# Kernel optimization log

Measured on AMD Instinct MI355X. Metric: run time of the kernel, lower is better.

## Reference

```python
import jax, jax.numpy as jnp
import numpy as np

K = 3          # kernel_size
PAD = K // 2   # unfold padding
BN_EPS = 1e-5


def _conv(x, w, dilation, pad):
    # x: [B,C,H,W], w: [O,I,kh,kw]
    return jax.lax.conv_general_dilated(
        x, w, window_strides=(1, 1), padding=[(pad, pad), (pad, pad)],
        rhs_dilation=(dilation, dilation),
        dimension_numbers=("NCHW", "OIHW", "NCHW"))


def _bn(x, g, b, rm, rv):
    # eval-mode batchnorm with running stats
    inv = g / jnp.sqrt(rv + BN_EPS)
    return x * inv[None, :, None, None] + (b - rm * inv)[None, :, None, None]


def setup_inputs() -> dict:
    key = jax.random.key(0)
    ks = jax.random.split(key, 8)
    B, T, H, W = 8, 5, 512, 512
    mid = 16  # max(16, T // 4)
    inp = {
        "x_aligned": jax.random.normal(ks[0], (B, T, H, W), jnp.float32),
        "raw_diff": jax.random.normal(ks[1], (B, T - 1, H, W), jnp.float32),
        "w1": jax.random.normal(ks[2], (mid, T, 3, 3), jnp.float32) * 0.1,
        "g1": jnp.ones((mid,), jnp.float32), "b1": jnp.zeros((mid,), jnp.float32),
        "rm1": jnp.zeros((mid,), jnp.float32), "rv1": jnp.ones((mid,), jnp.float32),
        "w2": jax.random.normal(ks[3], (mid, mid, 3, 3), jnp.float32) * 0.1,
        "g2": jnp.ones((mid,), jnp.float32), "b2": jnp.zeros((mid,), jnp.float32),
        "rm2": jnp.zeros((mid,), jnp.float32), "rv2": jnp.ones((mid,), jnp.float32),
        "w3": jax.random.normal(ks[4], (mid, mid, 3, 3), jnp.float32) * 0.1,
        "g3": jnp.ones((mid,), jnp.float32), "b3": jnp.zeros((mid,), jnp.float32),
        "rm3": jnp.zeros((mid,), jnp.float32), "rv3": jnp.ones((mid,), jnp.float32),
        "w4": jax.random.normal(ks[5], (T * K * K, mid, 1, 1), jnp.float32) * 0.1,
        "bias": jnp.full((1,), -1.0, jnp.float32),
    }
    return inp


def reference(x_aligned, raw_diff, w1, g1, b1, rm1, rv1, w2, g2, b2, rm2, rv2,
              w3, g3, b3, rm3, rv3, w4, bias):
    B, T, H, W = x_aligned.shape
    # _accumulate: sequential abs-add == sum of abs over frame-diff axis
    acc = jnp.sum(jnp.abs(raw_diff), axis=1, keepdims=True)  # [B,1,H,W]
    mean = jnp.mean(acc)
    n = acc.size
    std = jnp.sqrt(jnp.sum((acc - mean) ** 2) / (n - 1))  # unbiased (torch default)
    motion = (acc - mean) / (std + 1e-6)
    motion_seq = jnp.broadcast_to(motion, (B, T, H, W))
    # _generate_kernel: conv+BN+ReLU stack with dilations 1,2,4 then 1x1
    h = jax.nn.relu(_bn(_conv(motion_seq, w1, 1, 1), g1, b1, rm1, rv1))
    h = jax.nn.relu(_bn(_conv(h, w2, 2, 2), g2, b2, rm2, rv2))
    h = jax.nn.relu(_bn(_conv(h, w3, 4, 4), g3, b3, rm3, rv3))
    raw_kernel = _conv(h, w4, 1, 0).reshape(B, T, K * K, H, W)
    kernel = (jax.nn.sigmoid(raw_kernel + bias[0]) + 0.01) * 10.0
    # _enhance: unfold (KxK patches, zero pad) then per-pixel weighted sum
    xp = jnp.pad(x_aligned, ((0, 0), (0, 0), (PAD, PAD), (PAD, PAD)))
    patches = jnp.stack(
        [xp[:, :, i:i + H, j:j + W] for i in range(K) for j in range(K)],
        axis=2)  # [B,T,K*K,H,W], matches F.unfold row-major kernel order
    return jnp.sum(kernel * patches, axis=2)  # [B,T,H,W]
```

## Files before the change

kernel.cpp:

```cpp
#include <hip/hip_runtime.h>
#include <hip/hip_bf16.h>
#include <math.h>

#define HH 512
#define WW 512
#define BB 8
#define TT 5
#define MID 16
#define HWSZ (HH*WW)
#define NPIX (BB*HWSZ)

typedef __attribute__((ext_vector_type(8))) short bf16x8;
typedef __attribute__((ext_vector_type(4))) float f32x4;

__device__ inline unsigned short f2bf(float f){
  unsigned u = __float_as_uint(f);
  u = u + 0x7fffu + ((u >> 16) & 1u);
  return (unsigned short)(u >> 16);
}
__device__ inline unsigned packpair(float a, float b){
  unsigned ua = __float_as_uint(a) + 0x8000u;
  unsigned ub = __float_as_uint(b) + 0x8000u;
  return __builtin_amdgcn_perm(ub, ua, 0x07060302u);
}
__device__ inline float blo(unsigned u){ return __uint_as_float(u << 16); }
__device__ inline float bhi(unsigned u){ return __uint_as_float(u & 0xffff0000u); }

union U4B { uint4 u; bf16x8 h; };


__global__ __launch_bounds__(256) void k_acc(const float* __restrict__ rd,
                                             float4* __restrict__ acc,
                                             float2* __restrict__ partial){
  int t = blockIdx.x * 256 + threadIdx.x;
  int i = t << 2;
  int b = i >> 18, p = i & (HWSZ - 1);
  const float* base = rd + (size_t)b * 4 * HWSZ + p;
  float4 f0 = *(const float4*)(base);
  float4 f1 = *(const float4*)(base + HWSZ);
  float4 f2 = *(const float4*)(base + 2*HWSZ);
  float4 f3 = *(const float4*)(base + 3*HWSZ);
  float4 s4;
  s4.x = fabsf(f0.x) + fabsf(f1.x) + fabsf(f2.x) + fabsf(f3.x);
  s4.y = fabsf(f0.y) + fabsf(f1.y) + fabsf(f2.y) + fabsf(f3.y);
  s4.z = fabsf(f0.z) + fabsf(f1.z) + fabsf(f2.z) + fabsf(f3.z);
  s4.w = fabsf(f0.w) + fabsf(f1.w) + fabsf(f2.w) + fabsf(f3.w);
  acc[t] = s4;
  float s  = s4.x + s4.y + s4.z + s4.w;
  float s2 = s4.x*s4.x + s4.y*s4.y + s4.z*s4.z + s4.w*s4.w;
  #pragma unroll
  for (int off = 32; off; off >>= 1){
    s  += __shfl_down(s,  off);
    s2 += __shfl_down(s2, off);
  }
  __shared__ float ls[4], ls2[4];
  int lane = threadIdx.x & 63, wid = threadIdx.x >> 6;
  if (lane == 0){ ls[wid] = s; ls2[wid] = s2; }
  __syncthreads();
  if (threadIdx.x == 0)
    partial[blockIdx.x] = make_float2(ls[0]+ls[1]+ls[2]+ls[3],
                                      ls2[0]+ls2[1]+ls2[2]+ls2[3]);
}

__global__ __launch_bounds__(256) void k_prep(const float2* __restrict__ partial,
    const float* __restrict__ w1, const float* __restrict__ w2, const float* __restrict__ w3,
    const float* __restrict__ g1, const float* __restrict__ b1, const float* __restrict__ rm1, const float* __restrict__ rv1,
    const float* __restrict__ g2, const float* __restrict__ b2, const float* __restrict__ rm2, const float* __restrict__ rv2,
    const float* __restrict__ g3, const float* __restrict__ b3, const float* __restrict__ rm3, const float* __restrict__ rv3,
    const float* __restrict__ w4, const float* __restrict__ bias0,
    float* __restrict__ cst, unsigned* __restrict__ wsB2, unsigned* __restrict__ wsB3,
    uint4* __restrict__ wsB4){
  int t = threadIdx.x;
  double s = 0.0, s2 = 0.0;
  for (int j = t; j < 2048; j += 256){
    float2 v = partial[j];
    s += (double)v.x; s2 += (double)v.y;
  }
  #pragma unroll
  for (int off = 32; off; off >>= 1){
    s  += __shfl_down(s,  off);
    s2 += __shfl_down(s2, off);
  }
  __shared__ double ds[4], ds2[4];
  int lane = t & 63, wid = t >> 6;
  if (lane == 0){ ds[wid] = s; ds2[wid] = s2; }
  __syncthreads();
  if (t == 0){
    double S  = ds[0]+ds[1]+ds[2]+ds[3];
    double S2 = ds2[0]+ds2[1]+ds2[2]+ds2[3];
    double n = (double)NPIX;
    double mean = S / n;
    double var  = (S2 - n * mean * mean) / (n - 1.0);
    double sd   = sqrt(var);
    cst[0] = (float)mean;
    cst[1] = (float)(1.0 / (sd + 1e-6));
    cst[242] = bias0[0];
  }
  if (t < 144){
    int c = t / 9, k = t % 9;
    float sw = 0.f;
    for (int f = 0; f < TT; f++) sw += w1[c*45 + f*9 + k];
    cst[2 + t] = sw;
  }
  if (t < 16){
    float s1 = g1[t] * rsqrtf(rv1[t] + 1e-5f);
    cst[146 + t] = s1; cst[162 + t] = b1[t] - rm1[t] * s1;
    float c2 = g2[t] * rsqrtf(rv2[t] + 1e-5f);
    cst[288 + t] = c2; cst[304 + t] = b2[t] - rm2[t] * c2;
    float c3 = g3[t] * rsqrtf(rv3[t] + 1e-5f);
    cst[320 + t] = c3; cst[336 + t] = b3[t] - rm3[t] * c3;
  }
  for (int it = 0; it < 5; it++){
    int idx = it * 256 + t;
    int m = idx >> 8, rem = idx & 255;
    int L = rem >> 2, jj = rem & 3;
    int out = L & 15, q = L >> 4;
    unsigned v2 = 0, v3 = 0;
    #pragma unroll
    for (int h = 0; h < 2; h++){
      int j = 2*jj + h;
      int k = q*8 + j;
      int tap = 2*m + (k >> 4);
      int ci = k & 15;
      unsigned bv2 = 0, bv3 = 0;
      if (tap < 9){
        bv2 = f2bf(w2[out*144 + ci*9 + tap]);
        bv3 = f2bf(w3[out*144 + ci*9 + tap]);
      }
      v2 |= bv2 << (16*h);
      v3 |= bv3 << (16*h);
    }
    wsB2[idx] = v2; wsB3[idx] = v3;
  }
  if (t < 192){
    int c = t >> 6, L = t & 63;
    int n = L & 15, q = L >> 4;
    int o = c*16 + n;
    unsigned vv[4];
    #pragma unroll
    for (int jj = 0; jj < 4; jj++){
      unsigned pk = 0;
      #pragma unroll
      for (int h = 0; h < 2; h++){
        int j = 2*jj + h, kci = q*8 + j;
        unsigned bv = 0;
        if (kci < 16 && o < 45) bv = f2bf(w4[o*16 + kci]);
        pk |= bv << (16*h);
      }
      vv[jj] = pk;
    }
    wsB4[c*64 + L] = make_uint4(vv[0], vv[1], vv[2], vv[3]);
  }
}

__global__ __launch_bounds__(256) void k_conv1(const float* __restrict__ acc,
                                               const float* __restrict__ C,
                                               uint4* __restrict__ h1){
  int i = blockIdx.x * 256 + threadIdx.x;
  int b = i >> 18, p = i & (HWSZ - 1);
  int y = p >> 9, x = p & 511;
  float mean = C[0], inv = C[1];
  const float* ab = acc + ((size_t)b << 18);
  float a[MID];
  #pragma unroll
  for (int o = 0; o < MID; o++) a[o] = 0.f;
  #pragma unroll
  for (int ky = 0; ky < 3; ky++){
    int yy = y + ky - 1;
    if ((unsigned)yy >= HH) continue;
    #pragma unroll
    for (int kx = 0; kx < 3; kx++){
      int xx = x + kx - 1;
      if ((unsigned)xx >= WW) continue;
      float m = (ab[(yy << 9) + xx] - mean) * inv;
      int k = ky * 3 + kx;
      #pragma unroll
      for (int o = 0; o < MID; o++) a[o] = fmaf(C[2 + o*9 + k], m, a[o]);
    }
  }
  unsigned pk[8];
  #pragma unroll
  for (int j = 0; j < 8; j++){
    float v0 = fmaxf(0.f, fmaf(a[2*j],   C[146 + 2*j],   C[162 + 2*j]));
    float v1 = fmaxf(0.f, fmaf(a[2*j+1], C[146 + 2*j+1], C[162 + 2*j+1]));
    pk[j] = (unsigned)f2bf(v0) | ((unsigned)f2bf(v1) << 16);
  }
  uint4* dst = h1 + (size_t)i * 2;
  dst[0] = make_uint4(pk[0], pk[1], pk[2], pk[3]);
  dst[1] = make_uint4(pk[4], pk[5], pk[6], pk[7]);
}

template<int DIL>
__device__ inline f32x4 convW(const uint4* __restrict__ hin, const uint4 wfrag[5],
                              int b, int y, int x0, int col, int q, f32x4 cc){
  int chSel = q & 1;
  bool hiTap = (q >= 2);
  #pragma unroll
  for (int m = 0; m < 5; m++){
    const int ta = 2*m, tb = 2*m + 1;
    int dy = (hiTap ? tb/3 : ta/3) - 1;
    int dx = (hiTap ? tb%3 : ta%3) - 1;
    bool tv = hiTap ? (tb < 9) : true;
    int yy = y + dy * DIL;
    int xx = x0 + col + dx * DIL;
    bool valid = tv && ((unsigned)yy < HH) && ((unsigned)xx < WW);
    U4B a; a.u = make_uint4(0u, 0u, 0u, 0u);
    if (valid) a.u = hin[(((unsigned)((b << 18) | (yy << 9) | xx)) << 1) | (unsigned)chSel];
    U4B bb; bb.u = wfrag[m];
    cc = __builtin_amdgcn_mfma_f32_16x16x32_bf16(bb.h, a.h, cc, 0, 0, 0);
  }
  return cc;
}

__global__ __launch_bounds__(256) void k_conv2m(const uint4* __restrict__ h1,
                                                const float* __restrict__ C,
                                                const unsigned* __restrict__ wsB2,
                                                uint2* __restrict__ h2){
  int lane = threadIdx.x & 63, wv = threadIdx.x >> 6;
  int w = blockIdx.x * 4 + wv;
  int base = w << 6;
  int b = base >> 18, rem = base & (HWSZ - 1);
  int y = rem >> 9, wx = rem & 511;
  uint4 wfrag[5];
  #pragma unroll
  for (int m = 0; m < 5; m++) wfrag[m] = ((const uint4*)wsB2)[m*64 + lane];
  int col = lane & 15, q = lane >> 4;
  float4 sc = *(const float4*)&C[288 + q*4];
  float4 bi = *(const float4*)&C[304 + q*4];
  #pragma unroll
  for (int g = 0; g < 4; g++){
    f32x4 cc = {0.f, 0.f, 0.f, 0.f};
    cc = convW<2>(h1, wfrag, b, y, wx + g*16, col, q, cc);
    float v0 = fmaxf(0.f, fmaf(cc[0], sc.x, bi.x));
    float v1 = fmaxf(0.f, fmaf(cc[1], sc.y, bi.y));
    float v2 = fmaxf(0.f, fmaf(cc[2], sc.z, bi.z));
    float v3 = fmaxf(0.f, fmaf(cc[3], sc.w, bi.w));
    h2[(size_t)(base + g*16 + col)*4 + q] = make_uint2(packpair(v0, v1), packpair(v2, v3));
  }
}

__global__ __launch_bounds__(256) void k_conv3m(const uint4* __restrict__ h2,
                                                const float* __restrict__ C,
                                                const unsigned* __restrict__ wsB3,
                                                const uint4* __restrict__ wsB4,
                                                const float* __restrict__ xal,
                                                float* __restrict__ out){
  __shared__ uint4 LB[4][640];
  int lane = threadIdx.x & 63, wv = threadIdx.x >> 6;
  char* myL = (char*)LB[wv];
  unsigned short* Lk = (unsigned short*)(myL + 3072);
  int w = blockIdx.x * 4 + wv;
  int base = w << 6;
  int b = base >> 18, rem = base & (HWSZ - 1);
  int y = rem >> 9, wx = rem & 511;
  uint4 wfrag[5];
  #pragma unroll
  for (int m = 0; m < 5; m++) wfrag[m] = ((const uint4*)wsB3)[m*64 + lane];
  uint4 bw[3];
  #pragma unroll
  for (int c = 0; c < 3; c++) bw[c] = wsB4[c*64 + lane];
  int col = lane & 15, q = lane >> 4;
  float4 sc = *(const float4*)&C[320 + q*4];
  float4 bi = *(const float4*)&C[336 + q*4];
  float cb = C[242];

  #pragma unroll
  for (int g = 0; g < 4; g++){
    f32x4 cc = {0.f, 0.f, 0.f, 0.f};
    cc = convW<4>(h2, wfrag, b, y, wx + g*16, col, q, cc);
    float v0 = fmaxf(0.f, fmaf(cc[0], sc.x, bi.x));
    float v1 = fmaxf(0.f, fmaf(cc[1], sc.y, bi.y));
    float v2 = fmaxf(0.f, fmaf(cc[2], sc.z, bi.z));
    float v3 = fmaxf(0.f, fmaf(cc[3], sc.w, bi.w));
    *(uint2*)(myL + (g*16 + col)*48 + q*8) = make_uint2(packpair(v0, v1), packpair(v2, v3));

    U4B a; a.u = make_uint4(0u, 0u, 0u, 0u);
    if (q < 2) a.u = *(const uint4*)(myL + (g*16 + col)*48 + q*16);
    #pragma unroll
    for (int c = 0; c < 3; c++){
      f32x4 aw = {cb, cb, cb, cb};
      U4B bb; bb.u = bw[c];
      aw = __builtin_amdgcn_mfma_f32_16x16x32_bf16(a.h, bb.h, aw, 0, 0, 0);
      #pragma unroll
      for (int r = 0; r < 4; r++){
        float e  = __expf(-aw[r]);
        float rc = __builtin_amdgcn_rcpf(1.f + e);
        float kern = fmaf(10.f, rc, 0.1f);
        unsigned u = __float_as_uint(kern) + 0x8000u;
        Lk[(g*16 + q*4 + r)*56 + c*16 + col] = (unsigned short)(u >> 16);
      }
    }
  }

  unsigned kvf[24];
  {
    const uint4* kp = (const uint4*)(myL + 3072 + lane*112);
    #pragma unroll
    for (int jj = 0; jj < 6; jj++){
      uint4 u = kp[jj];
      kvf[4*jj] = u.x; kvf[4*jj+1] = u.y; kvf[4*jj+2] = u.z; kvf[4*jj+3] = u.w;
    }
  }
  int px = wx + lane;
  bool mxl = (px > 0), mxr = (px < 511), mym = (y > 0), myp = (y < 511);
  bool msk[9] = { mym&&mxl, mym, mym&&mxr,
                  mxl,      true, mxr,
                  myp&&mxl, myp, myp&&mxr };
  int rowm = mym ? -2048 : 0;
  int rowp = myp ?  2048 : 0;
  int loff = mxl ? -4 : 0;
  int roff = mxr ?  4 : 0;
  const char* base0 = (const char*)(xal + ((size_t)(b*TT) << 18) + (y << 9) + px);
  #pragma unroll
  for (int t = 0; t < TT; t++){
    const char* pc = base0 + (size_t)t * (HWSZ*4);
    const char* pm = pc + rowm;
    const char* pp = pc + rowp;
    float xv[9];
    xv[0] = *(const float*)(pm + loff);
    xv[1] = *(const float*)(pm);
    xv[2] = *(const float*)(pm + roff);
    xv[3] = *(const float*)(pc + loff);
    xv[4] = *(const float*)(pc);
    xv[5] = *(const float*)(pc + roff);
    xv[6] = *(const float*)(pp + loff);
    xv[7] = *(const float*)(pp);
    xv[8] = *(const float*)(pp + roff);
    float ov = 0.f;
    #pragma unroll
    for (int k = 0; k < 9; k++){
      int n = t*9 + k;
      unsigned u = kvf[n >> 1];
      float kf = (n & 1) ? bhi(u) : blo(u);
      float kern = msk[k] ? kf : 0.f;
      ov = fmaf(kern, xv[k], ov);
    }
    out[((size_t)(b*TT + t) << 18) + (y << 9) + px] = ov;
  }
}

extern "C" void kernel_launch(void* const* d_in, const int* in_sizes, int n_in,
                              void* d_out, int out_size, void* d_ws, size_t ws_size,
                              hipStream_t stream){
  const float* xal = (const float*)d_in[0];
  const float* rd  = (const float*)d_in[1];
  const float* w1  = (const float*)d_in[2];
  const float* g1  = (const float*)d_in[3];
  const float* b1  = (const float*)d_in[4];
  const float* rm1 = (const float*)d_in[5];
  const float* rv1 = (const float*)d_in[6];
  const float* w2  = (const float*)d_in[7];
  const float* g2  = (const float*)d_in[8];
  const float* b2  = (const float*)d_in[9];
  const float* rm2 = (const float*)d_in[10];
  const float* rv2 = (const float*)d_in[11];
  const float* w3  = (const float*)d_in[12];
  const float* g3  = (const float*)d_in[13];
  const float* b3  = (const float*)d_in[14];
  const float* rm3 = (const float*)d_in[15];
  const float* rv3 = (const float*)d_in[16];
  const float* w4  = (const float*)d_in[17];
  const float* bias= (const float*)d_in[18];
  float* out = (float*)d_out;

  char* ws = (char*)d_ws;
  float2*   partial = (float2*)ws;
  float*    cst   = (float*)(ws + 16384);
  unsigned* wsB2  = (unsigned*)(ws + 32768);
  unsigned* wsB3  = (unsigned*)(ws + 40960);
  uint4*    wsB4  = (uint4*)(ws + 49152);
  float*    acc   = (float*)(ws + 65536);
  uint4*    h1    = (uint4*)(ws + 65536 + (size_t)NPIX*4);
  char*     h2    = (char*)(ws + 65536 + (size_t)NPIX*4 + (size_t)NPIX*32);

  k_acc<<<2048, 256, 0, stream>>>(rd, (float4*)acc, partial);
  k_prep<<<1, 256, 0, stream>>>(partial, w1, w2, w3,
                                g1, b1, rm1, rv1,
                                g2, b2, rm2, rv2,
                                g3, b3, rm3, rv3, w4, bias, cst, wsB2, wsB3, wsB4);
  k_conv1<<<NPIX/256, 256, 0, stream>>>(acc, cst, h1);
  k_conv2m<<<NPIX/256, 256, 0, stream>>>(h1, cst, wsB2, (uint2*)h2);
  k_conv3m<<<NPIX/256, 256, 0, stream>>>((const uint4*)h2, cst, wsB3, wsB4, xal, out);
}
```

Baseline: 293.9 us.

## Fuse conv1 into conv2 via shared-memory halo tiles, dropping the h1 buffer

Merges the first 3x3 conv and the dilated second conv into one kernel. Each block computes conv1 for an 8x64 output tile plus a 2-pixel halo into LDS, then runs the MFMA dilation-2 conv from LDS. This removes the global write and read of the 32-byte-per-pixel h1 intermediate and one kernel launch. In exchange it recomputes conv1 on halo pixels (about 1.6x the work) and uses about 26 KB of LDS per block, which may limit occupancy.

Result: faster. 272.4 us (-7.3%).

```diff
diff --git a/kernel.cpp b/kernel.cpp
--- a/kernel.cpp
+++ b/kernel.cpp
@@ -153,41 +153,98 @@
   }
 }
 
-__global__ __launch_bounds__(256) void k_conv1(const float* __restrict__ acc,
-                                               const float* __restrict__ C,
-                                               uint4* __restrict__ h1){
-  int i = blockIdx.x * 256 + threadIdx.x;
-  int b = i >> 18, p = i & (HWSZ - 1);
-  int y = p >> 9, x = p & 511;
+#define TR 12
+#define TC 68
+__global__ __launch_bounds__(256) void k_conv12(const float* __restrict__ acc,
+                                                const float* __restrict__ C,
+                                                const unsigned* __restrict__ wsB2,
+                                                uint2* __restrict__ h2){
+  __shared__ uint4 PL[2][TR*TC];
+  int tid = threadIdx.x;
+  int blk = blockIdx.x;
+  int xt = blk & 7, yt = (blk >> 3) & 63, b = blk >> 9;
+  int y0 = yt << 3, x0 = xt << 6;
   float mean = C[0], inv = C[1];
   const float* ab = acc + ((size_t)b << 18);
-  float a[MID];
-  #pragma unroll
-  for (int o = 0; o < MID; o++) a[o] = 0.f;
-  #pragma unroll
-  for (int ky = 0; ky < 3; ky++){
-    int yy = y + ky - 1;
-    if ((unsigned)yy >= HH) continue;
-    #pragma unroll
-    for (int kx = 0; kx < 3; kx++){
-      int xx = x + kx - 1;
-      if ((unsigned)xx >= WW) continue;
-      float m = (ab[(yy << 9) + xx] - mean) * inv;
-      int k = ky * 3 + kx;
+  #pragma unroll
+  for (int it = 0; it < 4; it++){
+    int i = it*256 + tid;
+    if (i < TR*TC){
+      int r = (i * 241) >> 14;
+      int p = i - r*TC;
+      int gy = y0 - 2 + r, gx = x0 - 2 + p;
+      uint4 lo = make_uint4(0u,0u,0u,0u), hi = lo;
+      if ((unsigned)gy < HH && (unsigned)gx < WW){
+        float a[MID];
+        #pragma unroll
+        for (int o = 0; o < MID; o++) a[o] = 0.f;
+        #pragma unroll
+        for (int ky = 0; ky < 3; ky++){
+          int yy = gy + ky - 1;
+          if ((unsigned)yy >= HH) continue;
+          #pragma unroll
+          for (int kx = 0; kx < 3; kx++){
+            int xx = gx + kx - 1;
+            if ((unsigned)xx >= WW) continue;
+            float m = (ab[(yy << 9) + xx] - mean) * inv;
+            int k = ky * 3 + kx;
+            #pragma unroll
+            for (int o = 0; o < MID; o++) a[o] = fmaf(C[2 + o*9 + k], m, a[o]);
+          }
+        }
+        unsigned pk[8];
+        #pragma unroll
+        for (int j = 0; j < 8; j++){
+          float v0 = fmaxf(0.f, fmaf(a[2*j],   C[146 + 2*j],   C[162 + 2*j]));
+          float v1 = fmaxf(0.f, fmaf(a[2*j+1], C[146 + 2*j+1], C[162 + 2*j+1]));
+          pk[j] = packpair(v0, v1);
+        }
+        lo = make_uint4(pk[0], pk[1], pk[2], pk[3]);
+        hi = make_uint4(pk[4], pk[5], pk[6], pk[7]);
+      }
+      PL[0][r*TC + p] = lo;
+      PL[1][r*TC + p] = hi;
+    }
+  }
+  __syncthreads();
+  int lane = tid & 63, wv = tid >> 6;
+  int col = lane & 15, q = lane >> 4;
+  int chSel = q & 1;
+  bool hiTap = (q >= 2);
+  uint4 wfrag[5];
+  #pragma unroll
+  for (int m = 0; m < 5; m++) wfrag[m] = ((const uint4*)wsB2)[m*64 + lane];
+  float4 sc = *(const float4*)&C[288 + q*4];
+  float4 bi = *(const float4*)&C[304 + q*4];
+  #pragma unroll
+  for (int rr = 0; rr < 2; rr++){
+    int ly = wv*2 + rr;
+    #pragma unroll
+    for (int g = 0; g < 4; g++){
+      int lx = g << 4;
+      f32x4 cc = {0.f, 0.f, 0.f, 0.f};
       #pragma unroll
-      for (int o = 0; o < MID; o++) a[o] = fmaf(C[2 + o*9 + k], m, a[o]);
-    }
-  }
-  unsigned pk[8];
-  #pragma unroll
-  for (int j = 0; j < 8; j++){
-    float v0 = fmaxf(0.f, fmaf(a[2*j],   C[146 + 2*j],   C[162 + 2*j]));
-    float v1 = fmaxf(0.f, fmaf(a[2*j+1], C[146 + 2*j+1], C[162 + 2*j+1]));
-    pk[j] = (unsigned)f2bf(v0) | ((unsigned)f2bf(v1) << 16);
-  }
-  uint4* dst = h1 + (size_t)i * 2;
-  dst[0] = make_uint4(pk[0], pk[1], pk[2], pk[3]);
-  dst[1] = make_uint4(pk[4], pk[5], pk[6], pk[7]);
+      for (int m = 0; m < 5; m++){
+        const int ta = 2*m, tb = 2*m + 1;
+        int dy = (hiTap ? tb/3 : ta/3) - 1;
+        int dx = (hiTap ? tb%3 : ta%3) - 1;
+        bool tv = hiTap ? (tb < 9) : true;
+        int trow = ly + 2 + 2*dy;
+        int tpx  = lx + 2 + col + 2*dx;
+        U4B bv; bv.u = PL[chSel][trow*TC + tpx];
+        if (!tv) bv.u = make_uint4(0u,0u,0u,0u);
+        U4B wb; wb.u = wfrag[m];
+        cc = __builtin_amdgcn_mfma_f32_16x16x32_bf16(wb.h, bv.h, cc, 0, 0, 0);
+      }
+      float v0 = fmaxf(0.f, fmaf(cc[0], sc.x, bi.x));
+      float v1 = fmaxf(0.f, fmaf(cc[1], sc.y, bi.y));
+      float v2 = fmaxf(0.f, fmaf(cc[2], sc.z, bi.z));
+      float v3 = fmaxf(0.f, fmaf(cc[3], sc.w, bi.w));
+      int gy = y0 + ly, gx = x0 + lx + col;
+      h2[(size_t)((b << 18) | (gy << 9) | gx)*4 + q] =
+          make_uint2(packpair(v0, v1), packpair(v2, v3));
+    }
+  }
 }
 
 template<int DIL>
@@ -210,33 +267,6 @@
     cc = __builtin_amdgcn_mfma_f32_16x16x32_bf16(bb.h, a.h, cc, 0, 0, 0);
   }
   return cc;
-}
-
-__global__ __launch_bounds__(256) void k_conv2m(const uint4* __restrict__ h1,
-                                                const float* __restrict__ C,
-                                                const unsigned* __restrict__ wsB2,
-                                                uint2* __restrict__ h2){
-  int lane = threadIdx.x & 63, wv = threadIdx.x >> 6;
-  int w = blockIdx.x * 4 + wv;
-  int base = w << 6;
-  int b = base >> 18, rem = base & (HWSZ - 1);
-  int y = rem >> 9, wx = rem & 511;
-  uint4 wfrag[5];
-  #pragma unroll
-  for (int m = 0; m < 5; m++) wfrag[m] = ((const uint4*)wsB2)[m*64 + lane];
-  int col = lane & 15, q = lane >> 4;
-  float4 sc = *(const float4*)&C[288 + q*4];
-  float4 bi = *(const float4*)&C[304 + q*4];
-  #pragma unroll
-  for (int g = 0; g < 4; g++){
-    f32x4 cc = {0.f, 0.f, 0.f, 0.f};
-    cc = convW<2>(h1, wfrag, b, y, wx + g*16, col, q, cc);
-    float v0 = fmaxf(0.f, fmaf(cc[0], sc.x, bi.x));
-    float v1 = fmaxf(0.f, fmaf(cc[1], sc.y, bi.y));
-    float v2 = fmaxf(0.f, fmaf(cc[2], sc.z, bi.z));
-    float v3 = fmaxf(0.f, fmaf(cc[3], sc.w, bi.w));
-    h2[(size_t)(base + g*16 + col)*4 + q] = make_uint2(packpair(v0, v1), packpair(v2, v3));
-  }
 }
 
 __global__ __launch_bounds__(256) void k_conv3m(const uint4* __restrict__ h2,
@@ -370,15 +400,13 @@
   unsigned* wsB3  = (unsigned*)(ws + 40960);
   uint4*    wsB4  = (uint4*)(ws + 49152);
   float*    acc   = (float*)(ws + 65536);
-  uint4*    h1    = (uint4*)(ws + 65536 + (size_t)NPIX*4);
-  char*     h2    = (char*)(ws + 65536 + (size_t)NPIX*4 + (size_t)NPIX*32);
+  char*     h2    = (char*)(ws + 65536 + (size_t)NPIX*4);
 
   k_acc<<<2048, 256, 0, stream>>>(rd, (float4*)acc, partial);
   k_prep<<<1, 256, 0, stream>>>(partial, w1, w2, w3,
                                 g1, b1, rm1, rv1,
                                 g2, b2, rm2, rv2,
                                 g3, b3, rm3, rv3, w4, bias, cst, wsB2, wsB3, wsB4);
-  k_conv1<<<NPIX/256, 256, 0, stream>>>(acc, cst, h1);
-  k_conv2m<<<NPIX/256, 256, 0, stream>>>(h1, cst, wsB2, (uint2*)h2);
+  k_conv12<<<4096, 256, 0, stream>>>(acc, cst, wsB2, (uint2*)h2);
   k_conv3m<<<NPIX/256, 256, 0, stream>>>((const uint4*)h2, cst, wsB3, wsB4, xal, out);
 }
```
